# Performance work log

Measured on AMD Instinct MI355X. Metric: run time of the kernel, lower is better.

Reference implementation:

```python
import jax, jax.numpy as jnp
import numpy as np

B, T, C, H = 4, 2048, 1024, 128  # batch, block_size, n_embds, head_size


def setup_inputs() -> dict:
    key = jax.random.key(0)
    k1, k2, k3, k4 = jax.random.split(key, 4)
    x = jax.random.normal(k1, (B, T, C), dtype=jnp.float32)
    # Linear(n_embds, head_size, bias=False) weights, stored as [C, H] so q = x @ Wq
    s = C ** -0.5
    Wq = jax.random.normal(k2, (C, H), dtype=jnp.float32) * s
    Wk = jax.random.normal(k3, (C, H), dtype=jnp.float32) * s
    Wv = jax.random.normal(k4, (C, H), dtype=jnp.float32) * s
    return {"x": x, "Wq": Wq, "Wk": Wk, "Wv": Wv}


def reference(x, Wq, Wk, Wv):
    # q, k, v projections (no bias)
    q = x @ Wq  # [B, T, H]
    k = x @ Wk  # [B, T, H]
    v = x @ Wv  # [B, T, H]
    scale = q.shape[-1] ** -0.5
    wei = jnp.einsum('btd,bsd->bts', q, k) * scale  # [B, T, T]
    # causal mask: positions where tril == 0 (upper triangle) get -inf
    t = wei.shape[1]
    causal = jnp.tril(jnp.ones((t, t), dtype=bool))
    wei = jnp.where(causal, wei, -jnp.inf)
    # NOTE: source uses F.softmax(wei, dim=1) -> normalize over the QUERY axis
    wei = jax.nn.softmax(wei, axis=1)
    out = wei @ v  # [B, T, H]
    return out
```

## Files before the change

### kernel.cpp

```cpp
#include <hip/hip_runtime.h>
#include <math.h>

#define B_ 4
#define T_ 2048
#define C_ 1024
#define H_ 128
#define RCHUNK 128
#define NCHUNK (T_ / RCHUNK)
#define NSCH 32

typedef unsigned short u16;
typedef unsigned int   u32;
typedef short short8  __attribute__((ext_vector_type(8)));
typedef short short4v __attribute__((ext_vector_type(4)));
typedef float floatx4 __attribute__((ext_vector_type(4)));

__device__ __forceinline__ u16 f2bf(float f) {
    union { float f; u32 u; } v; v.f = f;
    return (u16)((v.u + 0x7fffu + ((v.u >> 16) & 1u)) >> 16);
}
__device__ __forceinline__ float bf2f(u16 h) {
    union { u32 u; float f; } v; v.u = ((u32)h) << 16;
    return v.f;
}

__global__ __launch_bounds__(256) void convert_w_kernel(
    const float* __restrict__ Wq, const float* __restrict__ Wk,
    const float* __restrict__ Wv, u16* __restrict__ Wt)
{
    const int k0 = blockIdx.x * 64, n0 = blockIdx.y * 64, widx = blockIdx.z;
    const float* W = (widx == 0) ? Wq : (widx == 1) ? Wk : Wv;

    __shared__ float ts[64][68];
    for (int i = threadIdx.x; i < 64 * 16; i += 256) {
        int r = i >> 4, c4 = i & 15;
        float4 v = *(const float4*)&W[(size_t)(k0 + r) * H_ + n0 + c4 * 4];
        ts[r][c4 * 4 + 0] = v.x; ts[r][c4 * 4 + 1] = v.y;
        ts[r][c4 * 4 + 2] = v.z; ts[r][c4 * 4 + 3] = v.w;
    }
    __syncthreads();
    for (int i = threadIdx.x; i < 64 * 16; i += 256) {
        int n = i >> 4, k4 = i & 15;
        short4v o;
        #pragma unroll
        for (int j = 0; j < 4; ++j) o[j] = (short)f2bf(ts[k4 * 4 + j][n]);
        *(short4v*)&Wt[(size_t)widx * H_ * C_ + (size_t)(n0 + n) * C_ + k0 + k4 * 4] = o;
    }
}

__global__ __launch_bounds__(256) void qkv_gemm_kernel(
    const float* __restrict__ x, const u16* __restrict__ Wt,
    u16* __restrict__ Qb, u16* __restrict__ Kb, u16* __restrict__ Vt)
{
    const int m0   = blockIdx.x * 64;
    const int widx = blockIdx.y;
    const u16* Wg = Wt + (size_t)widx * H_ * C_;

    __shared__ u16 As[64 * 136];
    __shared__ u16 Bs[128 * 136];

    const int w    = threadIdx.x >> 6;
    const int lane = threadIdx.x & 63;
    const int q    = lane >> 4, r = lane & 15;

    floatx4 acc[8] = {};

    for (int k0 = 0; k0 < C_; k0 += 128) {
        for (int i = threadIdx.x; i < 64 * 16; i += 256) {
            int rr = i >> 4, c = i & 15;
            const float* xg = &x[(size_t)(m0 + rr) * C_ + k0 + c * 8];
            float4 a = *(const float4*)xg;
            float4 b = *(const float4*)(xg + 4);
            short8 o;
            o[0]=(short)f2bf(a.x); o[1]=(short)f2bf(a.y);
            o[2]=(short)f2bf(a.z); o[3]=(short)f2bf(a.w);
            o[4]=(short)f2bf(b.x); o[5]=(short)f2bf(b.y);
            o[6]=(short)f2bf(b.z); o[7]=(short)f2bf(b.w);
            *(short8*)&As[rr * 136 + c * 8] = o;
        }
        for (int i = threadIdx.x; i < 128 * 16; i += 256) {
            int rr = i >> 4, c = i & 15;
            *(float4*)&Bs[rr * 136 + c * 8] =
                *(const float4*)&Wg[(size_t)rr * C_ + k0 + c * 8];
        }
        __syncthreads();

        #pragma unroll
        for (int kk = 0; kk < 4; ++kk) {
            short8 af = *(const short8*)&As[(16 * w + r) * 136 + kk * 32 + q * 8];
            #pragma unroll
            for (int nt = 0; nt < 8; ++nt) {
                short8 bf = *(const short8*)&Bs[(16 * nt + r) * 136 + kk * 32 + q * 8];
                acc[nt] = __builtin_amdgcn_mfma_f32_16x16x32_bf16(af, bf, acc[nt], 0, 0, 0);
            }
        }
        __syncthreads();
    }

    if (widx == 2) {
        const int bb  = m0 / T_;
        const int tt0 = (m0 - bb * T_) + 16 * w + q * 4;
        #pragma unroll
        for (int nt = 0; nt < 8; ++nt) {
            short4v o;
            #pragma unroll
            for (int reg = 0; reg < 4; ++reg) o[reg] = (short)f2bf(acc[nt][reg]);
            *(short4v*)&Vt[((size_t)bb * H_ + 16 * nt + r) * T_ + tt0] = o;
        }
    } else {
        u16* dst = (widx == 0) ? Qb : Kb;
        #pragma unroll
        for (int nt = 0; nt < 8; ++nt)
            #pragma unroll
            for (int reg = 0; reg < 4; ++reg) {
                int mm = m0 + 16 * w + q * 4 + reg;
                int nn = 16 * nt + r;
                dst[(size_t)mm * H_ + nn] = f2bf(acc[nt][reg]);
            }
    }
}

__global__ __launch_bounds__(256) void scores_kernel(
    const u16* __restrict__ Qb, const u16* __restrict__ Kb,
    u16* __restrict__ S, float* __restrict__ pm, float* __restrict__ pl)
{
    const int si = blockIdx.x;
    const int ti = blockIdx.y;
    const int b  = blockIdx.z;
    if (si > ti) return;
    const int t0 = ti * 128, s0 = si * 128;
    const bool diag = (si == ti);

    __shared__ u16 smem[2 * 128 * 136];
    u16* Qs = smem;
    u16* Ks = smem + 128 * 136;

    const u16* Qg = Qb + ((size_t)b * T_ + t0) * H_;
    const u16* Kg = Kb + ((size_t)b * T_ + s0) * H_;

    for (int i = threadIdx.x; i < 128 * 16; i += 256) {
        int rr = i >> 4, c = i & 15;
        *(float4*)&Qs[rr * 136 + c * 8] = *(const float4*)&Qg[(size_t)rr * H_ + c * 8];
        *(float4*)&Ks[rr * 136 + c * 8] = *(const float4*)&Kg[(size_t)rr * H_ + c * 8];
    }
    __syncthreads();

    const int w    = threadIdx.x >> 6;
    const int lane = threadIdx.x & 63;
    const int q    = lane >> 4, r = lane & 15;

    floatx4 acc[2][8] = {};
    #pragma unroll
    for (int kk = 0; kk < 4; ++kk) {
        short8 a0 = *(const short8*)&Qs[(32 * w +      r) * 136 + kk * 32 + q * 8];
        short8 a1 = *(const short8*)&Qs[(32 * w + 16 + r) * 136 + kk * 32 + q * 8];
        #pragma unroll
        for (int nt = 0; nt < 8; ++nt) {
            short8 bf = *(const short8*)&Ks[(16 * nt + r) * 136 + kk * 32 + q * 8];
            acc[0][nt] = __builtin_amdgcn_mfma_f32_16x16x32_bf16(a0, bf, acc[0][nt], 0, 0, 0);
            acc[1][nt] = __builtin_amdgcn_mfma_f32_16x16x32_bf16(a1, bf, acc[1][nt], 0, 0, 0);
        }
    }
    __syncthreads();

    u16*   tile = smem;
    float* redm = (float*)(smem + 128 * 136);
    float* redl = redm + 16 * 128;

    const float scale = 0.08838834764831845f;
    #pragma unroll
    for (int nt = 0; nt < 8; ++nt) {
        const int sl = 16 * nt + r;
        float v[8];  bool val[8];
        #pragma unroll
        for (int mt = 0; mt < 2; ++mt)
            #pragma unroll
            for (int reg = 0; reg < 4; ++reg) {
                const int j  = mt * 4 + reg;
                const int tl = 32 * w + 16 * mt + q * 4 + reg;
                v[j] = acc[mt][nt][reg] * scale;
                tile[tl * 136 + sl] = f2bf(v[j]);
                val[j] = (!diag) || (tl >= sl);
            }
        float mx = -INFINITY;
        #pragma unroll
        for (int j = 0; j < 8; ++j) mx = fmaxf(mx, val[j] ? v[j] : -INFINITY);
        float sm = 0.f;
        #pragma unroll
        for (int j = 0; j < 8; ++j) if (val[j]) sm += __expf(v[j] - mx);
        redm[(4 * w + q) * 128 + sl] = mx;
        redl[(4 * w + q) * 128 + sl] = sm;
    }
    __syncthreads();

    if (threadIdx.x < 128) {
        const int c = threadIdx.x;
        float M = -INFINITY;
        #pragma unroll
        for (int g = 0; g < 16; ++g) M = fmaxf(M, redm[g * 128 + c]);
        float L = 0.f;
        #pragma unroll
        for (int g = 0; g < 16; ++g) {
            float lg = redl[g * 128 + c];
            if (lg > 0.f) L += lg * __expf(redm[g * 128 + c] - M);
        }
        const size_t o = ((size_t)b * NCHUNK + ti) * T_ + s0 + c;
        pm[o] = M;
        pl[o] = L;
    }

    for (int i = threadIdx.x; i < 128 * 16; i += 256) {
        int tl = i >> 4, cc = (i >> 3) & 1, c8 = i & 7;
        u16* Sg = S + (((size_t)b * NSCH + 2 * si + cc) * T_ + t0 + tl) * 64;
        *(float4*)&Sg[c8 * 8] = *(float4*)&tile[tl * 136 + cc * 64 + c8 * 8];
    }
}

__global__ __launch_bounds__(256) void stats_reduce_kernel(
    const float* __restrict__ pm, const float* __restrict__ pl,
    float* __restrict__ m, float* __restrict__ linv)
{
    const int idx = blockIdx.x * 256 + threadIdx.x;
    const int b = idx >> 11, s = idx & (T_ - 1);
    const int c0 = s >> 7;

    float M = -INFINITY;
    for (int c = c0; c < NCHUNK; ++c)
        M = fmaxf(M, pm[((size_t)b * NCHUNK + c) * T_ + s]);

    float L = 0.f;
    for (int c = c0; c < NCHUNK; ++c) {
        float mc = pm[((size_t)b * NCHUNK + c) * T_ + s];
        float lc = pl[((size_t)b * NCHUNK + c) * T_ + s];
        if (lc > 0.f) L += lc * __expf(mc - M);
    }
    m[idx]    = M;
    linv[idx] = 1.0f / L;
}

#define RST 132
__global__ __launch_bounds__(512) void out_kernel(
    const u16* __restrict__ S, const u16* __restrict__ Vt,
    const float* __restrict__ m, const float* __restrict__ linv,
    float* __restrict__ out)
{
    const int b  = blockIdx.y;
    const int tb = (int)(gridDim.x - 1 - blockIdx.x);
    const int t0 = tb * 16;
    const int nchunks = (t0 + 79) >> 6;

    const int w    = threadIdx.x >> 6;
    const int lane = threadIdx.x & 63;
    const int q    = lane >> 4, r = lane & 15;
    const int t    = t0 + r;

    const u16*   SB  = S    + (size_t)b * NSCH * T_ * 64;
    const float* mB  = m    + (size_t)b * T_;
    const float* lB  = linv + (size_t)b * T_;
    const u16*   VtB = Vt   + (size_t)b * H_ * T_;

    floatx4 acc[8] = {};

    short8 sc[2];  float4 mc[2][2], lc[2][2];

    int ci = w;
    if (ci < nchunks) {
        const u16* Sc = SB + ((size_t)ci * T_ + t) * 64;
        const int  s0 = ci * 64;
        #pragma unroll
        for (int kk = 0; kk < 2; ++kk) {
            const int sl = kk * 32 + q * 8;
            sc[kk]    = *(const short8*)&Sc[sl];
            mc[kk][0] = *(const float4*)&mB[s0 + sl];
            mc[kk][1] = *(const float4*)&mB[s0 + sl + 4];
            lc[kk][0] = *(const float4*)&lB[s0 + sl];
            lc[kk][1] = *(const float4*)&lB[s0 + sl + 4];
        }
    }

    while (ci < nchunks) {
        const int s0 = ci * 64;
        const int cn = ci + 8;

        short8 sn[2];  float4 mn[2][2], ln[2][2];
        if (cn < nchunks) {
            const u16* Sc = SB + ((size_t)cn * T_ + t) * 64;
            const int  s0n = cn * 64;
            #pragma unroll
            for (int kk = 0; kk < 2; ++kk) {
                const int sl = kk * 32 + q * 8;
                sn[kk]    = *(const short8*)&Sc[sl];
                mn[kk][0] = *(const float4*)&mB[s0n + sl];
                mn[kk][1] = *(const float4*)&mB[s0n + sl + 4];
                ln[kk][0] = *(const float4*)&lB[s0n + sl];
                ln[kk][1] = *(const float4*)&lB[s0n + sl + 4];
            }
        }

        #pragma unroll
        for (int kk = 0; kk < 2; ++kk) {
            const int sb = s0 + kk * 32 + q * 8;
            float mv[8], lv[8];
            *(float4*)&mv[0] = mc[kk][0];  *(float4*)&mv[4] = mc[kk][1];
            *(float4*)&lv[0] = lc[kk][0];  *(float4*)&lv[4] = lc[kk][1];

            short8 af;
            #pragma unroll
            for (int j = 0; j < 8; ++j) {
                float wj = 0.f;
                if (sb + j <= t)
                    wj = __expf(bf2f((u16)sc[kk][j]) - mv[j]) * lv[j];
                af[j] = (short)f2bf(wj);
            }
            #pragma unroll
            for (int nt = 0; nt < 8; ++nt) {
                short8 bf = *(const short8*)&VtB[(size_t)(16 * nt + r) * T_ + sb];
                acc[nt] = __builtin_amdgcn_mfma_f32_16x16x32_bf16(af, bf, acc[nt], 0, 0, 0);
            }
        }

        #pragma unroll
        for (int kk = 0; kk < 2; ++kk) {
            sc[kk] = sn[kk];
            mc[kk][0] = mn[kk][0];  mc[kk][1] = mn[kk][1];
            lc[kk][0] = ln[kk][0];  lc[kk][1] = ln[kk][1];
        }
        ci = cn;
    }

    __shared__ float red[8][16 * RST];
    #pragma unroll
    for (int nt = 0; nt < 8; ++nt)
        #pragma unroll
        for (int reg = 0; reg < 4; ++reg)
            red[w][(q * 4 + reg) * RST + 16 * nt + r] = acc[nt][reg];
    __syncthreads();

    float* outB = out + ((size_t)b * T_ + t0) * H_;
    for (int i = threadIdx.x; i < 16 * 128; i += 512) {
        const int row = i >> 7, col = i & 127;
        float sum = 0.f;
        #pragma unroll
        for (int g = 0; g < 8; ++g) sum += red[g][row * RST + col];
        outB[i] = sum;
    }
}

extern "C" void kernel_launch(void* const* d_in, const int* in_sizes, int n_in,
                              void* d_out, int out_size, void* d_ws, size_t ws_size,
                              hipStream_t stream) {
    const float* x  = (const float*)d_in[0];
    const float* Wq = (const float*)d_in[1];
    const float* Wk = (const float*)d_in[2];
    const float* Wv = (const float*)d_in[3];
    float* out = (float*)d_out;

    u16*   S    = (u16*)d_ws;
    float* m    = (float*)(S + (size_t)B_ * T_ * T_);
    float* linv = m + (size_t)B_ * T_;
    u16*   Wt   = (u16*)(linv + (size_t)B_ * T_);
    u16*   Qb   = Wt + (size_t)3 * H_ * C_;
    u16*   Kb   = Qb + (size_t)B_ * T_ * H_;
    u16*   Vt   = Kb + (size_t)B_ * T_ * H_;

    float* pm = (float*)d_out;
    float* pl = pm + (size_t)B_ * NCHUNK * T_;

    convert_w_kernel  <<<dim3(C_ / 64, H_ / 64, 3),    dim3(256), 0, stream>>>(Wq, Wk, Wv, Wt);
    qkv_gemm_kernel   <<<dim3(B_ * T_ / 64, 3),        dim3(256), 0, stream>>>(x, Wt, Qb, Kb, Vt);
    scores_kernel     <<<dim3(16, 16, B_),             dim3(256), 0, stream>>>(Qb, Kb, S, pm, pl);
    stats_reduce_kernel<<<dim3(B_ * T_ / 256),         dim3(256), 0, stream>>>(pm, pl, m, linv);
    out_kernel        <<<dim3(T_ / 16, B_),            dim3(512), 0, stream>>>(S, Vt, m, linv, out);
}
```

Before: 169.9 us.

## Split out_kernel over head halves, interleave m/linv, drop manual prefetch

```diff
diff --git a/kernel.cpp b/kernel.cpp
--- a/kernel.cpp
+++ b/kernel.cpp
@@ -218,7 +218,7 @@
 
 __global__ __launch_bounds__(256) void stats_reduce_kernel(
     const float* __restrict__ pm, const float* __restrict__ pl,
-    float* __restrict__ m, float* __restrict__ linv)
+    float* __restrict__ ml)
 {
     const int idx = blockIdx.x * 256 + threadIdx.x;
     const int b = idx >> 11, s = idx & (T_ - 1);
@@ -234,19 +234,20 @@
         float lc = pl[((size_t)b * NCHUNK + c) * T_ + s];
         if (lc > 0.f) L += lc * __expf(mc - M);
     }
-    m[idx]    = M;
-    linv[idx] = 1.0f / L;
-}
-
-#define RST 132
-__global__ __launch_bounds__(512) void out_kernel(
+    ml[2 * idx]     = M;
+    ml[2 * idx + 1] = 1.0f / L;
+}
+
+#define RST2 68
+__global__ __launch_bounds__(512, 8) void out_kernel(
     const u16* __restrict__ S, const u16* __restrict__ Vt,
-    const float* __restrict__ m, const float* __restrict__ linv,
-    float* __restrict__ out)
-{
-    const int b  = blockIdx.y;
-    const int tb = (int)(gridDim.x - 1 - blockIdx.x);
-    const int t0 = tb * 16;
+    const float* __restrict__ ml, float* __restrict__ out)
+{
+    const int b   = blockIdx.y;
+    const int bid = (int)(gridDim.x - 1 - blockIdx.x);
+    const int tb  = bid >> 1;
+    const int hh  = bid & 1;
+    const int t0  = tb * 16;
     const int nchunks = (t0 + 79) >> 6;
 
     const int w    = threadIdx.x >> 6;
@@ -254,95 +255,59 @@
     const int q    = lane >> 4, r = lane & 15;
     const int t    = t0 + r;
 
-    const u16*   SB  = S    + (size_t)b * NSCH * T_ * 64;
-    const float* mB  = m    + (size_t)b * T_;
-    const float* lB  = linv + (size_t)b * T_;
-    const u16*   VtB = Vt   + (size_t)b * H_ * T_;
-
-    floatx4 acc[8] = {};
-
-    short8 sc[2];  float4 mc[2][2], lc[2][2];
-
-    int ci = w;
-    if (ci < nchunks) {
+    const u16*   SB  = S  + (size_t)b * NSCH * T_ * 64;
+    const float* mlB = ml + (size_t)2 * b * T_;
+    const u16*   VtB = Vt + ((size_t)b * H_ + hh * 64) * T_;
+
+    floatx4 acc[4] = {};
+
+    for (int ci = w; ci < nchunks; ci += 8) {
+        const int s0 = ci * 64;
         const u16* Sc = SB + ((size_t)ci * T_ + t) * 64;
-        const int  s0 = ci * 64;
-        #pragma unroll
-        for (int kk = 0; kk < 2; ++kk) {
-            const int sl = kk * 32 + q * 8;
-            sc[kk]    = *(const short8*)&Sc[sl];
-            mc[kk][0] = *(const float4*)&mB[s0 + sl];
-            mc[kk][1] = *(const float4*)&mB[s0 + sl + 4];
-            lc[kk][0] = *(const float4*)&lB[s0 + sl];
-            lc[kk][1] = *(const float4*)&lB[s0 + sl + 4];
-        }
-    }
-
-    while (ci < nchunks) {
-        const int s0 = ci * 64;
-        const int cn = ci + 8;
-
-        short8 sn[2];  float4 mn[2][2], ln[2][2];
-        if (cn < nchunks) {
-            const u16* Sc = SB + ((size_t)cn * T_ + t) * 64;
-            const int  s0n = cn * 64;
-            #pragma unroll
-            for (int kk = 0; kk < 2; ++kk) {
-                const int sl = kk * 32 + q * 8;
-                sn[kk]    = *(const short8*)&Sc[sl];
-                mn[kk][0] = *(const float4*)&mB[s0n + sl];
-                mn[kk][1] = *(const float4*)&mB[s0n + sl + 4];
-                ln[kk][0] = *(const float4*)&lB[s0n + sl];
-                ln[kk][1] = *(const float4*)&lB[s0n + sl + 4];
-            }
-        }
+        short8 sc0 = *(const short8*)&Sc[q * 8];
+        short8 sc1 = *(const short8*)&Sc[32 + q * 8];
 
         #pragma unroll
         for (int kk = 0; kk < 2; ++kk) {
             const int sb = s0 + kk * 32 + q * 8;
-            float mv[8], lv[8];
-            *(float4*)&mv[0] = mc[kk][0];  *(float4*)&mv[4] = mc[kk][1];
-            *(float4*)&lv[0] = lc[kk][0];  *(float4*)&lv[4] = lc[kk][1];
+            float mlv[16];
+            *(float4*)&mlv[0]  = *(const float4*)&mlB[2 * sb];
+            *(float4*)&mlv[4]  = *(const float4*)&mlB[2 * sb + 4];
+            *(float4*)&mlv[8]  = *(const float4*)&mlB[2 * sb + 8];
+            *(float4*)&mlv[12] = *(const float4*)&mlB[2 * sb + 12];
+            short8 scc = kk ? sc1 : sc0;
 
             short8 af;
             #pragma unroll
             for (int j = 0; j < 8; ++j) {
                 float wj = 0.f;
                 if (sb + j <= t)
-                    wj = __expf(bf2f((u16)sc[kk][j]) - mv[j]) * lv[j];
+                    wj = __expf(bf2f((u16)scc[j]) - mlv[2 * j]) * mlv[2 * j + 1];
                 af[j] = (short)f2bf(wj);
             }
             #pragma unroll
-            for (int nt = 0; nt < 8; ++nt) {
+            for (int nt = 0; nt < 4; ++nt) {
                 short8 bf = *(const short8*)&VtB[(size_t)(16 * nt + r) * T_ + sb];
                 acc[nt] = __builtin_amdgcn_mfma_f32_16x16x32_bf16(af, bf, acc[nt], 0, 0, 0);
             }
         }
-
-        #pragma unroll
-        for (int kk = 0; kk < 2; ++kk) {
-            sc[kk] = sn[kk];
-            mc[kk][0] = mn[kk][0];  mc[kk][1] = mn[kk][1];
-            lc[kk][0] = ln[kk][0];  lc[kk][1] = ln[kk][1];
-        }
-        ci = cn;
-    }
-
-    __shared__ float red[8][16 * RST];
+    }
+
+    __shared__ float red[8][16 * RST2];
     #pragma unroll
-    for (int nt = 0; nt < 8; ++nt)
+    for (int nt = 0; nt < 4; ++nt)
         #pragma unroll
         for (int reg = 0; reg < 4; ++reg)
-            red[w][(q * 4 + reg) * RST + 16 * nt + r] = acc[nt][reg];
-    __syncthreads();
-
-    float* outB = out + ((size_t)b * T_ + t0) * H_;
-    for (int i = threadIdx.x; i < 16 * 128; i += 512) {
-        const int row = i >> 7, col = i & 127;
+            red[w][(q * 4 + reg) * RST2 + 16 * nt + r] = acc[nt][reg];
+    __syncthreads();
+
+    float* outB = out + ((size_t)b * T_ + t0) * H_ + hh * 64;
+    for (int i = threadIdx.x; i < 16 * 64; i += 512) {
+        const int row = i >> 6, col = i & 63;
         float sum = 0.f;
         #pragma unroll
-        for (int g = 0; g < 8; ++g) sum += red[g][row * RST + col];
-        outB[i] = sum;
+        for (int g = 0; g < 8; ++g) sum += red[g][row * RST2 + col];
+        outB[(size_t)row * H_ + col] = sum;
     }
 }
 
@@ -356,9 +321,8 @@
     float* out = (float*)d_out;
 
     u16*   S    = (u16*)d_ws;
-    float* m    = (float*)(S + (size_t)B_ * T_ * T_);
-    float* linv = m + (size_t)B_ * T_;
-    u16*   Wt   = (u16*)(linv + (size_t)B_ * T_);
+    float* ml   = (float*)(S + (size_t)B_ * T_ * T_);
+    u16*   Wt   = (u16*)(ml + (size_t)2 * B_ * T_);
     u16*   Qb   = Wt + (size_t)3 * H_ * C_;
     u16*   Kb   = Qb + (size_t)B_ * T_ * H_;
     u16*   Vt   = Kb + (size_t)B_ * T_ * H_;
@@ -369,6 +333,6 @@
     convert_w_kernel  <<<dim3(C_ / 64, H_ / 64, 3),    dim3(256), 0, stream>>>(Wq, Wk, Wv, Wt);
     qkv_gemm_kernel   <<<dim3(B_ * T_ / 64, 3),        dim3(256), 0, stream>>>(x, Wt, Qb, Kb, Vt);
     scores_kernel     <<<dim3(16, 16, B_),             dim3(256), 0, stream>>>(Qb, Kb, S, pm, pl);
-    stats_reduce_kernel<<<dim3(B_ * T_ / 256),         dim3(256), 0, stream>>>(pm, pl, m, linv);
-    out_kernel        <<<dim3(T_ / 16, B_),            dim3(512), 0, stream>>>(S, Vt, m, linv, out);
-}
+    stats_reduce_kernel<<<dim3(B_ * T_ / 256),         dim3(256), 0, stream>>>(pm, pl, ml);
+    out_kernel        <<<dim3(T_ / 16 * 2, B_),        dim3(512), 0, stream>>>(S, Vt, ml, out);
+}
```

After: 189.2 us. 11.3% more time.
